# Optimization experiments

Hardware: AMD Instinct MI355X
Metric: run time of the kernel (lower is better)

Reference implementation:

```python
import jax, jax.numpy as jnp
import numpy as np

NUM_KNNS = 200
TEMPERATURE = 0.07
NUM_CLASSES = 1000


def setup_inputs() -> dict:
    key = jax.random.key(0)
    k1, k2, k3, k4 = jax.random.split(key, 4)
    N, D, K = 1024, 512, 65536
    # features and queue are L2-normalized (queue init is normal_l2)
    features = jax.random.normal(k1, (N, D), jnp.float32)
    features = features / jnp.linalg.norm(features, axis=-1, keepdims=True)
    queue_features = jax.random.normal(k2, (K, D), jnp.float32)
    queue_features = queue_features / jnp.linalg.norm(queue_features, axis=-1, keepdims=True)
    labels = jax.random.randint(k3, (N,), 0, NUM_CLASSES, dtype=jnp.int32)
    queue_labels = jax.random.randint(k4, (K,), 0, NUM_CLASSES, dtype=jnp.int32)
    return {
        "features": features,
        "queue_features": queue_features,
        "labels": labels,
        "queue_labels": queue_labels,
        "queue_ptr": 0,
    }


def reference(features, queue_features, labels, queue_labels, queue_ptr):
    # --- kNN accuracy ---
    # similarity matmul: [N, K]
    sim = jnp.einsum('nd,kd->nk', features, queue_features)
    sim_weight, sim_indices = jax.lax.top_k(sim, k=NUM_KNNS)  # [N, k]
    sim_weight = jnp.exp(sim_weight / TEMPERATURE)
    # gather neighbor labels (equivalent to the one-hot einsum in the original)
    sim_labels = queue_labels[sim_indices]  # [N, k] int32
    one_hot_labels = jax.nn.one_hot(sim_labels, NUM_CLASSES, dtype=sim_weight.dtype)  # [N, k, C]
    pred_scores = jnp.sum(one_hot_labels * sim_weight[..., None], axis=1)  # [N, C]
    pred_labels = jnp.argmax(pred_scores, axis=-1)
    accuracy = jnp.mean((pred_labels == labels).astype(jnp.float32))

    # --- circular queue scatter update ---
    N = features.shape[0]
    K = queue_features.shape[0]
    inds = jnp.arange(N) + queue_ptr
    new_queue_features = queue_features.at[inds].set(features)
    new_queue_labels = queue_labels.at[inds].set(labels)
    new_queue_ptr = (queue_ptr + N) % K
    return accuracy, new_queue_features, new_queue_labels, new_queue_ptr
```

## Files before the change

kernel.cpp:

```cpp
#include <hip/hip_runtime.h>
#include <math.h>

#define N_ROWS 1024
#define DIM    512
#define KQ     65536
#define KNN    200
#define NCLS   1000
#define NBINS  4096
#define CAP    2048
#define INV_T  14.285714285714286f

typedef unsigned short u16;
typedef __attribute__((ext_vector_type(8))) short short8;
typedef __attribute__((ext_vector_type(4))) float f32x4;
struct alignas(8) U16x4 { u16 x, y, z, w; };

#define GLOAD_LDS16(g, l)                                               \
    __builtin_amdgcn_global_load_lds(                                   \
        (__attribute__((address_space(1))) void*)(g),                   \
        (__attribute__((address_space(3))) void*)(l), 16, 0, 0)

__device__ __forceinline__ void split1(float x, u16& h, u16& l) {
    unsigned u = __float_as_uint(x);
    unsigned hr = (u + 0x7FFFu + ((u >> 16) & 1u)) >> 16;
    float hf = __uint_as_float(hr << 16);
    float lo = x - hf;
    unsigned ul = __float_as_uint(lo);
    unsigned lr = (ul + 0x7FFFu + ((ul >> 16) & 1u)) >> 16;
    h = (u16)hr; l = (u16)lr;
}

#define QF_BLOCKS (KQ * DIM / 4 / 256)
#define FT_BLOCKS (N_ROWS * DIM / 4 / 256)

__global__ __launch_bounds__(256) void fused_update_split_kernel(
    const float* __restrict__ feats, const float* __restrict__ qf,
    const int* __restrict__ labels, const int* __restrict__ ql,
    const int* __restrict__ qptr,
    float* __restrict__ out_qf, float* __restrict__ out_ql,
    float* __restrict__ out_ptr,
    u16* __restrict__ Bhi, u16* __restrict__ Blo,
    u16* __restrict__ Ahi, u16* __restrict__ Alo) {
    int ptr = qptr[0];
    int b = blockIdx.x;
    if (b < QF_BLOCKS) {
        size_t t = (size_t)b * 256 + threadIdx.x;
        size_t idx = t * 4;
        int row = (int)(idx >> 9);
        int col = (int)(idx & 511);
        float4 v = *(const float4*)(qf + idx);
        U16x4 h, l;
        split1(v.x, h.x, l.x); split1(v.y, h.y, l.y);
        split1(v.z, h.z, l.z); split1(v.w, h.w, l.w);
        *(U16x4*)(Bhi + idx) = h;
        *(U16x4*)(Blo + idx) = l;
        int d = row - ptr; if (d < 0) d += KQ;
        float4 o = (d < N_ROWS) ? *(const float4*)(feats + (size_t)d * DIM + col) : v;
        *(float4*)(out_qf + idx) = o;
        if (col == 0)
            out_ql[row] = (float)((d < N_ROWS) ? labels[d] : ql[row]);
    } else {
        size_t t = (size_t)(b - QF_BLOCKS) * 256 + threadIdx.x;
        size_t idx = t * 4;
        float4 v = *(const float4*)(feats + idx);
        U16x4 h, l;
        split1(v.x, h.x, l.x); split1(v.y, h.y, l.y);
        split1(v.z, h.z, l.z); split1(v.w, h.w, l.w);
        *(U16x4*)(Ahi + idx) = h;
        *(U16x4*)(Alo + idx) = l;
        if (t == 0) out_ptr[0] = (float)((ptr + N_ROWS) % KQ);
    }
}

__global__ __launch_bounds__(256, 4) void gemm_mfma_kernel(
    const u16* __restrict__ Ahi, const u16* __restrict__ Alo,
    const u16* __restrict__ Bhi, const u16* __restrict__ Blo,
    float* __restrict__ C) {
    __shared__ u16 sA[2][128 * 32];
    __shared__ u16 sB[2][128 * 32];

    int tid = threadIdx.x;
    int wave = tid >> 6, lane = tid & 63;
    int q = lane >> 4, r = lane & 15;
    int bn = blockIdx.x, bm = blockIdx.y;
    int wm = wave & 1, wn = wave >> 1;

    const u16* gplane = (wave == 0) ? Ahi : (wave == 1) ? Alo
                      : (wave == 2) ? Bhi : Blo;
    int prow0 = (wave < 2) ? bm * 128 : bn * 128;
    const u16* gbase = gplane + (size_t)prow0 * DIM;
    u16* lbase = (wave == 0) ? sA[0] : (wave == 1) ? sA[1]
               : (wave == 2) ? sB[0] : sB[1];
    int lrow = lane >> 2;
    int lchunk = lane & 3;

    f32x4 acc[4][4] = {};

    for (int kt = 0; kt < DIM; kt += 32) {
        __syncthreads();
#pragma unroll
        for (int s = 0; s < 8; ++s) {
            const u16* g = gbase + (size_t)(s * 16 + lrow) * DIM + kt + lchunk * 8;
            GLOAD_LDS16(g, lbase + s * 512);
        }
        __syncthreads();

        short8 fa[2][4], fb[2][4];
#pragma unroll
        for (int t = 0; t < 4; ++t) {
            int am = wm * 64 + t * 16 + r;
            fa[0][t] = *(const short8*)&sA[0][am * 32 + q * 8];
            fa[1][t] = *(const short8*)&sA[1][am * 32 + q * 8];
            int bn_ = wn * 64 + t * 16 + r;
            fb[0][t] = *(const short8*)&sB[0][bn_ * 32 + q * 8];
            fb[1][t] = *(const short8*)&sB[1][bn_ * 32 + q * 8];
        }
#pragma unroll
        for (int i = 0; i < 4; ++i)
#pragma unroll
            for (int j = 0; j < 4; ++j) {
                acc[i][j] = __builtin_amdgcn_mfma_f32_16x16x32_bf16(
                    fa[0][i], fb[0][j], acc[i][j], 0, 0, 0);
                acc[i][j] = __builtin_amdgcn_mfma_f32_16x16x32_bf16(
                    fa[0][i], fb[1][j], acc[i][j], 0, 0, 0);
                acc[i][j] = __builtin_amdgcn_mfma_f32_16x16x32_bf16(
                    fa[1][i], fb[0][j], acc[i][j], 0, 0, 0);
            }
    }

#pragma unroll
    for (int i = 0; i < 4; ++i)
#pragma unroll
        for (int j = 0; j < 4; ++j)
#pragma unroll
            for (int g = 0; g < 4; ++g) {
                int row = bm * 128 + wm * 64 + i * 16 + q * 4 + g;
                int col = bn * 128 + wn * 64 + j * 16 + r;
                C[(size_t)row * KQ + col] = acc[i][j][g];
            }
}

#define LSTR 68
#define LA(k, m) ((k) * LSTR + (m))

__global__ __launch_bounds__(256) void gemm_nt_kernel(
    const float* __restrict__ A, const float* __restrict__ B,
    float* __restrict__ C) {
    __shared__ float As[32 * LSTR];
    __shared__ float Bs[32 * LSTR];
    int tid = threadIdx.x;
    int bn = blockIdx.x, bm = blockIdx.y;
    int tx = tid & 15, ty = tid >> 4;
    int lm = tid >> 3;
    int lk = (tid & 7) * 4;
    const float* Ab = A + (size_t)bm * 64 * DIM;
    const float* Bb = B + (size_t)bn * 64 * DIM;
    float acc[4][4] = {};
    for (int kt = 0; kt < DIM; kt += 32) {
        float4 a0 = *(const float4*)(Ab + (size_t)lm * DIM + kt + lk);
        float4 a1 = *(const float4*)(Ab + (size_t)(lm + 32) * DIM + kt + lk);
        float4 b0 = *(const float4*)(Bb + (size_t)lm * DIM + kt + lk);
        float4 b1 = *(const float4*)(Bb + (size_t)(lm + 32) * DIM + kt + lk);
        __syncthreads();
        As[LA(lk + 0, lm)] = a0.x;  As[LA(lk + 1, lm)] = a0.y;
        As[LA(lk + 2, lm)] = a0.z;  As[LA(lk + 3, lm)] = a0.w;
        As[LA(lk + 0, lm + 32)] = a1.x;  As[LA(lk + 1, lm + 32)] = a1.y;
        As[LA(lk + 2, lm + 32)] = a1.z;  As[LA(lk + 3, lm + 32)] = a1.w;
        Bs[LA(lk + 0, lm)] = b0.x;  Bs[LA(lk + 1, lm)] = b0.y;
        Bs[LA(lk + 2, lm)] = b0.z;  Bs[LA(lk + 3, lm)] = b0.w;
        Bs[LA(lk + 0, lm + 32)] = b1.x;  Bs[LA(lk + 1, lm + 32)] = b1.y;
        Bs[LA(lk + 2, lm + 32)] = b1.z;  Bs[LA(lk + 3, lm + 32)] = b1.w;
        __syncthreads();
#pragma unroll
        for (int kk = 0; kk < 32; ++kk) {
            float4 av = *(const float4*)&As[LA(kk, ty * 4)];
            float4 bv = *(const float4*)&Bs[LA(kk, tx * 4)];
            float a_[4] = {av.x, av.y, av.z, av.w};
            float b_[4] = {bv.x, bv.y, bv.z, bv.w};
#pragma unroll
            for (int i = 0; i < 4; ++i)
#pragma unroll
                for (int j = 0; j < 4; ++j) acc[i][j] += a_[i] * b_[j];
        }
    }
    for (int i = 0; i < 4; ++i) {
        float4 o = make_float4(acc[i][0], acc[i][1], acc[i][2], acc[i][3]);
        *(float4*)(C + (size_t)(bm * 64 + ty * 4 + i) * KQ + bn * 64 + tx * 4) = o;
    }
}

__device__ __forceinline__ unsigned order_key(float v) {
    unsigned u = __float_as_uint(v);
    return u ^ ((u & 0x80000000u) ? 0xFFFFFFFFu : 0x80000000u);
}

__global__ __launch_bounds__(1024) void topk_kernel(
    const float* __restrict__ sim, int r0,
    const int* __restrict__ ql, const int* __restrict__ labels,
    float* __restrict__ flags) {
    __shared__ unsigned hist[NBINS];
    __shared__ unsigned psum[1024];
    __shared__ float cval[CAP];
    __shared__ int   cidx[CAP];
    __shared__ float scores[NCLS];
    __shared__ float rbest[1024];
    __shared__ int   rcls[1024];
    __shared__ int   s_bstar, s_ncand;

    int row = blockIdx.x;
    int tid = threadIdx.x;
    const float4* s4 = (const float4*)(sim + (size_t)row * KQ);

    hist[tid] = 0; hist[tid + 1024] = 0; hist[tid + 2048] = 0; hist[tid + 3072] = 0;
    if (tid == 0) s_ncand = 0;
    __syncthreads();

    for (int i4 = tid; i4 < KQ / 4; i4 += 1024) {
        float4 v = s4[i4];
        atomicAdd(&hist[order_key(v.x) >> 20], 1u);
        atomicAdd(&hist[order_key(v.y) >> 20], 1u);
        atomicAdd(&hist[order_key(v.z) >> 20], 1u);
        atomicAdd(&hist[order_key(v.w) >> 20], 1u);
    }
    __syncthreads();

    unsigned loc = hist[4 * tid] + hist[4 * tid + 1] +
                   hist[4 * tid + 2] + hist[4 * tid + 3];
    psum[tid] = loc;
    __syncthreads();
    for (int off = 1; off < 1024; off <<= 1) {
        unsigned add = (tid + off < 1024) ? psum[tid + off] : 0u;
        __syncthreads();
        psum[tid] += add;
        __syncthreads();
    }
    unsigned running = psum[tid] - loc;
    for (int j = 3; j >= 0; --j) {
        unsigned c = hist[4 * tid + j];
        if (running < KNN && running + c >= KNN) s_bstar = 4 * tid + j;
        running += c;
    }
    __syncthreads();
    int bstar = s_bstar;

    for (int i4 = tid; i4 < KQ / 4; i4 += 1024) {
        float4 v = s4[i4];
        float vv[4] = {v.x, v.y, v.z, v.w};
#pragma unroll
        for (int c = 0; c < 4; ++c) {
            if ((int)(order_key(vv[c]) >> 20) >= bstar) {
                int p = atomicAdd(&s_ncand, 1);
                if (p < CAP) { cval[p] = vv[c]; cidx[p] = i4 * 4 + c; }
            }
        }
    }
    if (tid < NCLS) scores[tid] = 0.f;
    __syncthreads();

    int M = s_ncand; if (M > CAP) M = CAP;
    for (int c = tid; c < M; c += 1024) {
        float v = cval[c]; int id = cidx[c];
        int rank = 0;
        for (int j = 0; j < M; ++j) {
            float vj = cval[j];
            if (vj > v || (vj == v && cidx[j] < id)) rank++;
        }
        if (rank < KNN) {
            float w = expf(v * INV_T);
            atomicAdd(&scores[ql[id]], w);
        }
    }
    __syncthreads();

    float best = -1.f; int bc = 0;
    if (tid < NCLS) { best = scores[tid]; bc = tid; }
    rbest[tid] = best; rcls[tid] = bc;
    __syncthreads();
    for (int off = 512; off; off >>= 1) {
        if (tid < off) {
            float ob = rbest[tid + off]; int oc = rcls[tid + off];
            if (ob > rbest[tid] || (ob == rbest[tid] && oc < rcls[tid])) {
                rbest[tid] = ob; rcls[tid] = oc;
            }
        }
        __syncthreads();
    }
    if (tid == 0)
        flags[r0 + row] = (rcls[0] == labels[r0 + row]) ? 1.0f : 0.0f;
}

__global__ __launch_bounds__(256) void acc_kernel(
    const float* __restrict__ flags, float* __restrict__ out) {
    __shared__ float r[256];
    int tid = threadIdx.x;
    r[tid] = flags[tid] + flags[tid + 256] + flags[tid + 512] + flags[tid + 768];
    __syncthreads();
    for (int off = 128; off; off >>= 1) {
        if (tid < off) r[tid] += r[tid + off];
        __syncthreads();
    }
    if (tid == 0) out[0] = r[0] * (1.0f / 1024.0f);
}

extern "C" void kernel_launch(void* const* d_in, const int* in_sizes, int n_in,
                              void* d_out, int out_size, void* d_ws, size_t ws_size,
                              hipStream_t stream) {
    const float* feats  = (const float*)d_in[0];
    const float* qf     = (const float*)d_in[1];
    const int*   labels = (const int*)d_in[2];
    const int*   ql     = (const int*)d_in[3];
    const int*   qptr   = (const int*)d_in[4];

    float* out     = (float*)d_out;
    float* out_qf  = out + 1;
    float* out_ql  = out_qf + (size_t)KQ * DIM;
    float* out_ptr = out_ql + KQ;

    const size_t bplane = (size_t)KQ * DIM;
    const size_t aplane = (size_t)N_ROWS * DIM;

    int CH = 0;
    for (int c = 256; c >= 128; c >>= 1) {
        size_t need = 2 * bplane * 2 + 2 * aplane * 2 +
                      (size_t)c * KQ * 4 + N_ROWS * 4;
        if (need <= ws_size) { CH = c; break; }
    }

    if (CH > 0) {
        u16* Bhi = (u16*)d_ws;
        u16* Blo = Bhi + bplane;
        u16* Ahi = Blo + bplane;
        u16* Alo = Ahi + aplane;
        float* sim   = (float*)(Alo + aplane);
        float* flags = sim + (size_t)CH * KQ;

        fused_update_split_kernel<<<QF_BLOCKS + FT_BLOCKS, 256, 0, stream>>>(
            feats, qf, labels, ql, qptr, out_qf, out_ql, out_ptr,
            Bhi, Blo, Ahi, Alo);

        int nchunks = N_ROWS / CH;
        for (int c = 0; c < nchunks; ++c) {
            dim3 g(KQ / 128, CH / 128);
            gemm_mfma_kernel<<<g, 256, 0, stream>>>(
                Ahi + (size_t)c * CH * DIM, Alo + (size_t)c * CH * DIM,
                Bhi, Blo, sim);
            topk_kernel<<<CH, 1024, 0, stream>>>(sim, c * CH, ql, labels, flags);
        }
        acc_kernel<<<1, 256, 0, stream>>>(flags, out);
    } else {
        {
            long long total4 = (long long)KQ * DIM / 4;
        }
        int CHf = 256;
        while (CHf > 64 &&
               ((size_t)CHf * KQ * sizeof(float) + N_ROWS * sizeof(float)) > ws_size)
            CHf >>= 1;
        float* sim   = (float*)d_ws;
        float* flags = (float*)((char*)d_ws + (size_t)CHf * KQ * sizeof(float));
        fused_update_split_kernel<<<QF_BLOCKS + FT_BLOCKS, 256, 0, stream>>>(
            feats, qf, labels, ql, qptr, out_qf, out_ql, out_ptr,
            (u16*)sim, (u16*)sim, (u16*)sim, (u16*)sim);
        int nchunks = N_ROWS / CHf;
        for (int c = 0; c < nchunks; ++c) {
            const float* A = feats + (size_t)c * CHf * DIM;
            dim3 g(KQ / 64, CHf / 64);
            gemm_nt_kernel<<<g, 256, 0, stream>>>(A, qf, sim);
            topk_kernel<<<CHf, 1024, 0, stream>>>(sim, c * CHf, ql, labels, flags);
        }
        acc_kernel<<<1, 256, 0, stream>>>(flags, out);
    }
}
```

Baseline: 677.5 us.

## Estimate top-k threshold from a sample and rank only boundary-bin candidates

The top-k kernel now builds a coarse histogram from a strided sample of 1024 values to choose a conservative cutoff bin. It then makes a single pass over the row that collects candidates and builds their histogram together, where it previously needed two full passes. Candidates in bins strictly above the exact threshold bin are scored directly, and only the boundary bin gets the quadratic pairwise ranking, which replaces an O(M^2) rank over up to 2048 candidates. A fallback reruns the original full-histogram path if the sample yields too few or too many candidates, and the ranking for the boundary bin is capped at 256 entries.

```diff
diff --git a/kernel.cpp b/kernel.cpp
--- a/kernel.cpp
+++ b/kernel.cpp
@@ -7,7 +7,9 @@
 #define KNN    200
 #define NCLS   1000
 #define NBINS  4096
-#define CAP    2048
+#define CAP    3072
+#define CAP2   256
+#define SMIN   16
 #define INV_T  14.285714285714286f
 
 typedef unsigned short u16;
@@ -202,73 +204,142 @@
     __shared__ unsigned psum[1024];
     __shared__ float cval[CAP];
     __shared__ int   cidx[CAP];
+    __shared__ float cv2[CAP2];
+    __shared__ int   ci2[CAP2];
     __shared__ float scores[NCLS];
     __shared__ float rbest[1024];
     __shared__ int   rcls[1024];
-    __shared__ int   s_bstar, s_ncand;
+    __shared__ int   s_b0, s_bstar, s_above, s_ncand, s_n2, s_fb;
 
     int row = blockIdx.x;
     int tid = threadIdx.x;
-    const float4* s4 = (const float4*)(sim + (size_t)row * KQ);
+    const float* srow = sim + (size_t)row * KQ;
+    const float4* s4 = (const float4*)srow;
 
     hist[tid] = 0; hist[tid + 1024] = 0; hist[tid + 2048] = 0; hist[tid + 3072] = 0;
-    if (tid == 0) s_ncand = 0;
-    __syncthreads();
-
-    for (int i4 = tid; i4 < KQ / 4; i4 += 1024) {
-        float4 v = s4[i4];
-        atomicAdd(&hist[order_key(v.x) >> 20], 1u);
-        atomicAdd(&hist[order_key(v.y) >> 20], 1u);
-        atomicAdd(&hist[order_key(v.z) >> 20], 1u);
-        atomicAdd(&hist[order_key(v.w) >> 20], 1u);
-    }
-    __syncthreads();
-
-    unsigned loc = hist[4 * tid] + hist[4 * tid + 1] +
-                   hist[4 * tid + 2] + hist[4 * tid + 3];
-    psum[tid] = loc;
-    __syncthreads();
-    for (int off = 1; off < 1024; off <<= 1) {
-        unsigned add = (tid + off < 1024) ? psum[tid + off] : 0u;
-        __syncthreads();
-        psum[tid] += add;
-        __syncthreads();
-    }
-    unsigned running = psum[tid] - loc;
-    for (int j = 3; j >= 0; --j) {
-        unsigned c = hist[4 * tid + j];
-        if (running < KNN && running + c >= KNN) s_bstar = 4 * tid + j;
-        running += c;
-    }
-    __syncthreads();
-    int bstar = s_bstar;
+    if (tid == 0) { s_ncand = 0; s_n2 = 0; s_fb = 0; }
+    if (tid < NCLS) scores[tid] = 0.f;
+    __syncthreads();
+
+    atomicAdd(&hist[order_key(srow[tid * 64]) >> 20], 1u);
+    __syncthreads();
+    {
+        unsigned loc = hist[4 * tid] + hist[4 * tid + 1] +
+                       hist[4 * tid + 2] + hist[4 * tid + 3];
+        psum[tid] = loc;
+        __syncthreads();
+        for (int off = 1; off < 1024; off <<= 1) {
+            unsigned add = (tid + off < 1024) ? psum[tid + off] : 0u;
+            __syncthreads();
+            psum[tid] += add;
+            __syncthreads();
+        }
+        unsigned running = psum[tid] - loc;
+        for (int j = 3; j >= 0; --j) {
+            unsigned c = hist[4 * tid + j];
+            if (running < SMIN && running + c >= SMIN) s_b0 = 4 * tid + j;
+            running += c;
+        }
+    }
+    __syncthreads();
+    int b0 = s_b0;
+    hist[tid] = 0; hist[tid + 1024] = 0; hist[tid + 2048] = 0; hist[tid + 3072] = 0;
+    __syncthreads();
 
     for (int i4 = tid; i4 < KQ / 4; i4 += 1024) {
         float4 v = s4[i4];
         float vv[4] = {v.x, v.y, v.z, v.w};
 #pragma unroll
         for (int c = 0; c < 4; ++c) {
-            if ((int)(order_key(vv[c]) >> 20) >= bstar) {
+            int bin = (int)(order_key(vv[c]) >> 20);
+            if (bin >= b0) {
+                atomicAdd(&hist[bin], 1u);
                 int p = atomicAdd(&s_ncand, 1);
                 if (p < CAP) { cval[p] = vv[c]; cidx[p] = i4 * 4 + c; }
             }
         }
     }
-    if (tid < NCLS) scores[tid] = 0.f;
-    __syncthreads();
+    __syncthreads();
+    if (tid == 0 && (s_ncand < KNN || s_ncand > CAP)) s_fb = 1;
+    __syncthreads();
+
+    if (s_fb) {
+        hist[tid] = 0; hist[tid + 1024] = 0; hist[tid + 2048] = 0; hist[tid + 3072] = 0;
+        __syncthreads();
+        for (int i4 = tid; i4 < KQ / 4; i4 += 1024) {
+            float4 v = s4[i4];
+            atomicAdd(&hist[order_key(v.x) >> 20], 1u);
+            atomicAdd(&hist[order_key(v.y) >> 20], 1u);
+            atomicAdd(&hist[order_key(v.z) >> 20], 1u);
+            atomicAdd(&hist[order_key(v.w) >> 20], 1u);
+        }
+        __syncthreads();
+    }
+
+    {
+        unsigned loc = hist[4 * tid] + hist[4 * tid + 1] +
+                       hist[4 * tid + 2] + hist[4 * tid + 3];
+        psum[tid] = loc;
+        __syncthreads();
+        for (int off = 1; off < 1024; off <<= 1) {
+            unsigned add = (tid + off < 1024) ? psum[tid + off] : 0u;
+            __syncthreads();
+            psum[tid] += add;
+            __syncthreads();
+        }
+        unsigned running = psum[tid] - loc;
+        for (int j = 3; j >= 0; --j) {
+            unsigned c = hist[4 * tid + j];
+            if (running < KNN && running + c >= KNN) {
+                s_bstar = 4 * tid + j;
+                s_above = (int)running;
+            }
+            running += c;
+        }
+    }
+    __syncthreads();
+    int bstar = s_bstar;
+    int above = s_above;
+
+    if (s_fb) {
+        if (tid == 0) s_ncand = 0;
+        __syncthreads();
+        for (int i4 = tid; i4 < KQ / 4; i4 += 1024) {
+            float4 v = s4[i4];
+            float vv[4] = {v.x, v.y, v.z, v.w};
+#pragma unroll
+            for (int c = 0; c < 4; ++c) {
+                if ((int)(order_key(vv[c]) >> 20) >= bstar) {
+                    int p = atomicAdd(&s_ncand, 1);
+                    if (p < CAP) { cval[p] = vv[c]; cidx[p] = i4 * 4 + c; }
+                }
+            }
+        }
+        __syncthreads();
+    }
 
     int M = s_ncand; if (M > CAP) M = CAP;
     for (int c = tid; c < M; c += 1024) {
-        float v = cval[c]; int id = cidx[c];
+        float v = cval[c];
+        int bin = (int)(order_key(v) >> 20);
+        if (bin > bstar) {
+            atomicAdd(&scores[ql[cidx[c]]], expf(v * INV_T));
+        } else if (bin == bstar) {
+            int p = atomicAdd(&s_n2, 1);
+            if (p < CAP2) { cv2[p] = v; ci2[p] = cidx[c]; }
+        }
+    }
+    __syncthreads();
+
+    int n2 = s_n2; if (n2 > CAP2) n2 = CAP2;
+    for (int c = tid; c < n2; c += 1024) {
+        float v = cv2[c]; int id = ci2[c];
         int rank = 0;
-        for (int j = 0; j < M; ++j) {
-            float vj = cval[j];
-            if (vj > v || (vj == v && cidx[j] < id)) rank++;
-        }
-        if (rank < KNN) {
-            float w = expf(v * INV_T);
-            atomicAdd(&scores[ql[id]], w);
-        }
+        for (int j = 0; j < n2; ++j) {
+            float vj = cv2[j];
+            if (vj > v || (vj == v && ci2[j] < id)) rank++;
+        }
+        if (above + rank < KNN) atomicAdd(&scores[ql[id]], expf(v * INV_T));
     }
     __syncthreads();
 
@@ -348,9 +419,6 @@
         }
         acc_kernel<<<1, 256, 0, stream>>>(flags, out);
     } else {
-        {
-            long long total4 = (long long)KQ * DIM / 4;
-        }
         int CHf = 256;
         while (CHf > 64 &&
                ((size_t)CHf * KQ * sizeof(float) + N_ROWS * sizeof(float)) > ws_size)
```

After: 687.8 us. Within noise of the previous version (+1.5%).
